# Performance work log

Hardware: AMD Instinct MI355X
Metric: run time of the kernel (lower is better)

Reference implementation:

```python
import jax, jax.numpy as jnp
import numpy as np

SCALE = 1.0 / 7.0
EPS = 1e-7


def _pair_iou(b1, b2):
    """Elementwise IoU of cxcywh boxes, faithful to Loss.bboxs_iou (incl. eps placement)."""
    b1x1 = b1[..., 0] - b1[..., 2] * 0.5
    b1x2 = b1[..., 0] + b1[..., 2] * 0.5
    b1y1 = b1[..., 1] - b1[..., 3] * 0.5
    b1y2 = b1[..., 1] + b1[..., 3] * 0.5
    b2x1 = b2[..., 0] - b2[..., 2] * 0.5
    b2x2 = b2[..., 0] + b2[..., 2] * 0.5
    b2y1 = b2[..., 1] - b2[..., 3] * 0.5
    b2y2 = b2[..., 1] + b2[..., 3] * 0.5
    iw = jnp.maximum(jnp.minimum(b1x2, b2x2) - jnp.maximum(b1x1, b2x1), 0.0)
    ih = jnp.maximum(jnp.minimum(b1y2, b2y2) - jnp.maximum(b1y1, b2y1), 0.0)
    inter = iw * ih + EPS
    w1 = b1x2 - b1x1
    h1 = b1y2 - b1y1 + EPS
    w2 = b2x2 - b2x1
    h2 = b2y2 - b2y1 + EPS
    union = w1 * h1 + w2 * h2 - inter + EPS
    return inter / union


def _msum(mask, sq):
    return jnp.sum(jnp.where(mask, sq, 0.0))


def _forward(pre, target):
    B = pre.shape[0]
    pre = pre.reshape(B, 7, 7, 30)
    cell_obj = target[..., 4] > 0       # (B,7,7) grid cells with an object
    cell_noobj = target[..., 4] == 0    # (B,7,7) empty cells

    t_box = target[..., :10].reshape(B, 7, 7, 2, 5)
    p_box = pre[..., :10].reshape(B, 7, 7, 2, 5)

    # per-cell, per-box IoU(pred_b, target_b), b in {0,1}  -> (B,7,7,2)
    iou = _pair_iou(p_box[..., :4], t_box[..., :4])
    resp = jnp.argmax(iou, axis=-1)      # responsible box index (first max, like torch)
    nonresp = jnp.argmin(iou, axis=-1)   # non-responsible box index (first min)

    box_idx = jnp.arange(2)[None, None, None, :]       # (1,1,1,2)
    is_resp = box_idx == resp[..., None]               # (B,7,7,2)
    is_nonresp = box_idx == nonresp[..., None]

    # loop effect 1: zero the confidence of the non-responsible TARGET box
    new_conf = jnp.where(is_nonresp, 0.0, t_box[..., 4])   # (B,7,7,2)

    # loop effect 2: responsible target xy <- normalized offset of the *min-index* box's xy
    xy_nr = jnp.take_along_axis(t_box[..., :2], nonresp[..., None, None], axis=3)  # (B,7,7,1,2)
    xy_nr = xy_nr[..., 0, :]                                                        # (B,7,7,2)
    fxy = (xy_nr - (jnp.ceil(xy_nr / SCALE) - 1.0) * SCALE) / SCALE                 # (B,7,7,2)
    new_xy = jnp.where(is_resp[..., None], fxy[:, :, :, None, :], t_box[..., :2])   # (B,7,7,2,2)

    m_resp = is_resp & cell_obj[..., None]        # responsible boxes of object cells
    m_noresp = (~is_resp) & cell_obj[..., None]   # nomse mask (init 1, cleared at resp)

    loss_xy = _msum(m_resp[..., None], (p_box[..., :2] - new_xy) ** 2)
    loss_wh = _msum(m_resp[..., None],
                    (jnp.sqrt(p_box[..., 2:4] + EPS) - jnp.sqrt(t_box[..., 2:4] + EPS)) ** 2)
    loss_conf = _msum(m_resp, (p_box[..., 4] - new_conf) ** 2)
    loss_noconf = (_msum(m_noresp, (p_box[..., 4] - new_conf) ** 2)
                   + _msum(cell_noobj[..., None], (p_box[..., 4] - t_box[..., 4]) ** 2))
    loss_class = _msum(cell_obj[..., None], (pre[..., 10:] - target[..., 10:]) ** 2)

    loss = 5.0 * (loss_xy + loss_wh) + loss_class + loss_conf + 0.5 * loss_noconf
    return loss / jnp.float32(B)


def setup_inputs() -> dict:
    key = jax.random.key(0)
    k1, k2, k3 = jax.random.split(key, 3)
    B = 16384
    pre = jax.random.uniform(k1, (B, 7 * 7 * 30), dtype=jnp.float32)
    target = jax.random.uniform(k2, (B, 7, 7, 30), dtype=jnp.float32)
    # objectness in {0,1} on both box conf channels so obj/no-obj branches are exercised
    obj = (jax.random.uniform(k3, (B, 7, 7)) > 0.5).astype(jnp.float32)
    target = target.at[..., 4].set(obj).at[..., 9].set(obj)
    return {"pre": pre, "target": target}


def reference(pre, target):
    return _forward(pre, target)
```

## Files before the change

kernel.cpp:

```cpp
#include <hip/hip_runtime.h>

#define EPSF 1e-7f
#define SCALEF (1.0f / 7.0f)

__device__ __forceinline__ float pair_iou(const float* b1, const float* b2) {
    float b1x1 = b1[0] - b1[2] * 0.5f, b1x2 = b1[0] + b1[2] * 0.5f;
    float b1y1 = b1[1] - b1[3] * 0.5f, b1y2 = b1[1] + b1[3] * 0.5f;
    float b2x1 = b2[0] - b2[2] * 0.5f, b2x2 = b2[0] + b2[2] * 0.5f;
    float b2y1 = b2[1] - b2[3] * 0.5f, b2y2 = b2[1] + b2[3] * 0.5f;
    float iw = fmaxf(fminf(b1x2, b2x2) - fmaxf(b1x1, b2x1), 0.0f);
    float ih = fmaxf(fminf(b1y2, b2y2) - fmaxf(b1y1, b2y1), 0.0f);
    float inter = iw * ih + EPSF;
    float w1 = b1x2 - b1x1, h1 = b1y2 - b1y1 + EPSF;
    float w2 = b2x2 - b2x1, h2 = b2y2 - b2y1 + EPSF;
    float uni = w1 * h1 + w2 * h2 - inter + EPSF;
    return inter / uni;
}

__global__ __launch_bounds__(256) void yolo_loss_partial(
        const float* __restrict__ pre, const float* __restrict__ targ,
        float* __restrict__ partial, int n_cells) {
    int cell = blockIdx.x * 256 + threadIdx.x;
    float loss = 0.0f;
    if (cell < n_cells) {
        float p[30], t[30];
        const float2* p2 = reinterpret_cast<const float2*>(pre + (size_t)cell * 30);
        const float2* t2 = reinterpret_cast<const float2*>(targ + (size_t)cell * 30);
#pragma unroll
        for (int i = 0; i < 15; ++i) { float2 v = p2[i]; p[2 * i] = v.x; p[2 * i + 1] = v.y; }
#pragma unroll
        for (int i = 0; i < 15; ++i) { float2 v = t2[i]; t[2 * i] = v.x; t[2 * i + 1] = v.y; }

        bool cell_obj   = t[4] > 0.0f;
        bool cell_noobj = t[4] == 0.0f;

        float iou0 = pair_iou(p + 0, t + 0);
        float iou1 = pair_iou(p + 5, t + 5);
        int resp    = (iou1 > iou0) ? 1 : 0;
        int nonresp = (iou1 < iou0) ? 1 : 0;

        float xnr = nonresp ? t[5] : t[0];
        float ynr = nonresp ? t[6] : t[1];
        float fx = (xnr - (ceilf(xnr / SCALEF) - 1.0f) * SCALEF) / SCALEF;
        float fy = (ynr - (ceilf(ynr / SCALEF) - 1.0f) * SCALEF) / SCALEF;

        float lxy = 0.0f, lwh = 0.0f, lconf = 0.0f, lnoconf = 0.0f, lclass = 0.0f;
#pragma unroll
        for (int i = 0; i < 2; ++i) {
            const float* pb = p + i * 5;
            const float* tb = t + i * 5;
            bool is_resp    = (i == resp);
            bool is_nonresp = (i == nonresp);
            float new_conf = is_nonresp ? 0.0f : tb[4];
            if (cell_obj) {
                if (is_resp) {
                    float dx = pb[0] - fx, dy = pb[1] - fy;
                    lxy += dx * dx + dy * dy;
                    float dw = sqrtf(pb[2] + EPSF) - sqrtf(tb[2] + EPSF);
                    float dh = sqrtf(pb[3] + EPSF) - sqrtf(tb[3] + EPSF);
                    lwh += dw * dw + dh * dh;
                    float dc = pb[4] - new_conf;
                    lconf += dc * dc;
                } else {
                    float dc = pb[4] - new_conf;
                    lnoconf += dc * dc;
                }
            }
            if (cell_noobj) {
                float dc = pb[4] - tb[4];
                lnoconf += dc * dc;
            }
        }
        if (cell_obj) {
#pragma unroll
            for (int k = 10; k < 30; ++k) { float d = p[k] - t[k]; lclass += d * d; }
        }
        loss = 5.0f * (lxy + lwh) + lclass + lconf + 0.5f * lnoconf;
    }

#pragma unroll
    for (int off = 32; off > 0; off >>= 1) loss += __shfl_down(loss, off, 64);
    __shared__ float ssum[4];
    int lane = threadIdx.x & 63, wid = threadIdx.x >> 6;
    if (lane == 0) ssum[wid] = loss;
    __syncthreads();
    if (threadIdx.x == 0) partial[blockIdx.x] = ssum[0] + ssum[1] + ssum[2] + ssum[3];
}

__global__ __launch_bounds__(256) void yolo_loss_final(
        const float* __restrict__ partial, int n, float invB, float* __restrict__ out) {
    float v = 0.0f;
    for (int i = threadIdx.x; i < n; i += 256) v += partial[i];
#pragma unroll
    for (int off = 32; off > 0; off >>= 1) v += __shfl_down(v, off, 64);
    __shared__ float ssum[4];
    int lane = threadIdx.x & 63, wid = threadIdx.x >> 6;
    if (lane == 0) ssum[wid] = v;
    __syncthreads();
    if (threadIdx.x == 0) out[0] = (ssum[0] + ssum[1] + ssum[2] + ssum[3]) * invB;
}

extern "C" void kernel_launch(void* const* d_in, const int* in_sizes, int n_in,
                              void* d_out, int out_size, void* d_ws, size_t ws_size,
                              hipStream_t stream) {
    const float* pre  = (const float*)d_in[0];
    const float* targ = (const float*)d_in[1];
    float* out = (float*)d_out;
    float* partial = (float*)d_ws;

    int B = in_sizes[0] / 1470;
    int n_cells = B * 49;
    int nblocks = (n_cells + 255) / 256;

    yolo_loss_partial<<<nblocks, 256, 0, stream>>>(pre, targ, partial, n_cells);
    yolo_loss_final<<<1, 256, 0, stream>>>(partial, nblocks, 1.0f / (float)B, out);
}
```

Baseline: 44.33 us.

## Stage cells through LDS with coalesced float4 loads and split box/class work

Each block copies 128 cells of pred and target into shared memory with coalesced float4 loads, two chunks per block. Half the threads then compute the box/IoU terms and the other half the class term, which balances work and cuts per-thread registers. The aim is to replace strided per-thread float2 global loads (stride of 120 bytes) with fully coalesced transfers. The bounds check is removed and the grid is floor-divided, which assumes n_cells is a multiple of 256. That holds for B=16384 but is not a general guarantee.

```diff
diff --git a/kernel.cpp b/kernel.cpp
--- a/kernel.cpp
+++ b/kernel.cpp
@@ -19,72 +19,110 @@
 
 __global__ __launch_bounds__(256) void yolo_loss_partial(
         const float* __restrict__ pre, const float* __restrict__ targ,
-        float* __restrict__ partial, int n_cells) {
-    int cell = blockIdx.x * 256 + threadIdx.x;
-    float loss = 0.0f;
-    if (cell < n_cells) {
-        float p[30], t[30];
-        const float2* p2 = reinterpret_cast<const float2*>(pre + (size_t)cell * 30);
-        const float2* t2 = reinterpret_cast<const float2*>(targ + (size_t)cell * 30);
+        float* __restrict__ partial) {
+    __shared__ float4 s4[1920];
+    float* sp = reinterpret_cast<float*>(s4);
+    float* st = reinterpret_cast<float*>(s4 + 960);
+    const int tid = threadIdx.x;
+    float acc = 0.0f;
+
 #pragma unroll
-        for (int i = 0; i < 15; ++i) { float2 v = p2[i]; p[2 * i] = v.x; p[2 * i + 1] = v.y; }
+    for (int chunk = 0; chunk < 2; ++chunk) {
+        const size_t base = ((size_t)blockIdx.x * 256 + chunk * 128) * 30;
+        const float4* gp = reinterpret_cast<const float4*>(pre + base);
+        const float4* gt = reinterpret_cast<const float4*>(targ + base);
+        float4* sp4 = s4;
+        float4* st4 = s4 + 960;
 #pragma unroll
-        for (int i = 0; i < 15; ++i) { float2 v = t2[i]; t[2 * i] = v.x; t[2 * i + 1] = v.y; }
+        for (int k = 0; k < 3; ++k) {
+            int idx = tid + 256 * k;
+            sp4[idx] = gp[idx];
+            st4[idx] = gt[idx];
+        }
+        {
+            int idx = tid + 768;
+            if (idx < 960) { sp4[idx] = gp[idx]; st4[idx] = gt[idx]; }
+        }
+        __syncthreads();
 
-        bool cell_obj   = t[4] > 0.0f;
-        bool cell_noobj = t[4] == 0.0f;
-
-        float iou0 = pair_iou(p + 0, t + 0);
-        float iou1 = pair_iou(p + 5, t + 5);
-        int resp    = (iou1 > iou0) ? 1 : 0;
-        int nonresp = (iou1 < iou0) ? 1 : 0;
-
-        float xnr = nonresp ? t[5] : t[0];
-        float ynr = nonresp ? t[6] : t[1];
-        float fx = (xnr - (ceilf(xnr / SCALEF) - 1.0f) * SCALEF) / SCALEF;
-        float fy = (ynr - (ceilf(ynr / SCALEF) - 1.0f) * SCALEF) / SCALEF;
-
-        float lxy = 0.0f, lwh = 0.0f, lconf = 0.0f, lnoconf = 0.0f, lclass = 0.0f;
+        const int half = tid >> 7;
+        const int c = tid & 127;
+        const float* cp = sp + c * 30;
+        const float* ct = st + c * 30;
+        float loss = 0.0f;
+        if (half == 0) {
+            float p[10], t[10];
+            const float2* cp2 = reinterpret_cast<const float2*>(cp);
+            const float2* ct2 = reinterpret_cast<const float2*>(ct);
 #pragma unroll
-        for (int i = 0; i < 2; ++i) {
-            const float* pb = p + i * 5;
-            const float* tb = t + i * 5;
-            bool is_resp    = (i == resp);
-            bool is_nonresp = (i == nonresp);
-            float new_conf = is_nonresp ? 0.0f : tb[4];
-            if (cell_obj) {
-                if (is_resp) {
-                    float dx = pb[0] - fx, dy = pb[1] - fy;
-                    lxy += dx * dx + dy * dy;
-                    float dw = sqrtf(pb[2] + EPSF) - sqrtf(tb[2] + EPSF);
-                    float dh = sqrtf(pb[3] + EPSF) - sqrtf(tb[3] + EPSF);
-                    lwh += dw * dw + dh * dh;
-                    float dc = pb[4] - new_conf;
-                    lconf += dc * dc;
-                } else {
-                    float dc = pb[4] - new_conf;
+            for (int i = 0; i < 5; ++i) {
+                float2 a = cp2[i]; p[2 * i] = a.x; p[2 * i + 1] = a.y;
+                float2 b = ct2[i]; t[2 * i] = b.x; t[2 * i + 1] = b.y;
+            }
+            bool cell_obj   = t[4] > 0.0f;
+            bool cell_noobj = t[4] == 0.0f;
+            float iou0 = pair_iou(p + 0, t + 0);
+            float iou1 = pair_iou(p + 5, t + 5);
+            int resp    = (iou1 > iou0) ? 1 : 0;
+            int nonresp = (iou1 < iou0) ? 1 : 0;
+            float xnr = nonresp ? t[5] : t[0];
+            float ynr = nonresp ? t[6] : t[1];
+            float fx = (xnr - (ceilf(xnr / SCALEF) - 1.0f) * SCALEF) / SCALEF;
+            float fy = (ynr - (ceilf(ynr / SCALEF) - 1.0f) * SCALEF) / SCALEF;
+            float lxy = 0.0f, lwh = 0.0f, lconf = 0.0f, lnoconf = 0.0f;
+#pragma unroll
+            for (int i = 0; i < 2; ++i) {
+                const float* pb = p + i * 5;
+                const float* tb = t + i * 5;
+                bool is_resp    = (i == resp);
+                bool is_nonresp = (i == nonresp);
+                float new_conf = is_nonresp ? 0.0f : tb[4];
+                if (cell_obj) {
+                    if (is_resp) {
+                        float dx = pb[0] - fx, dy = pb[1] - fy;
+                        lxy += dx * dx + dy * dy;
+                        float dw = sqrtf(pb[2] + EPSF) - sqrtf(tb[2] + EPSF);
+                        float dh = sqrtf(pb[3] + EPSF) - sqrtf(tb[3] + EPSF);
+                        lwh += dw * dw + dh * dh;
+                        float dc = pb[4] - new_conf;
+                        lconf += dc * dc;
+                    } else {
+                        float dc = pb[4] - new_conf;
+                        lnoconf += dc * dc;
+                    }
+                }
+                if (cell_noobj) {
+                    float dc = pb[4] - tb[4];
                     lnoconf += dc * dc;
                 }
             }
-            if (cell_noobj) {
-                float dc = pb[4] - tb[4];
-                lnoconf += dc * dc;
+            loss = 5.0f * (lxy + lwh) + lconf + 0.5f * lnoconf;
+        } else {
+            float tobj = ct[4];
+            if (tobj > 0.0f) {
+                float s = 0.0f;
+                const float2* cp2 = reinterpret_cast<const float2*>(cp + 10);
+                const float2* ct2 = reinterpret_cast<const float2*>(ct + 10);
+#pragma unroll
+                for (int i = 0; i < 10; ++i) {
+                    float2 a = cp2[i], b = ct2[i];
+                    float d0 = a.x - b.x, d1 = a.y - b.y;
+                    s += d0 * d0 + d1 * d1;
+                }
+                loss = s;
             }
         }
-        if (cell_obj) {
-#pragma unroll
-            for (int k = 10; k < 30; ++k) { float d = p[k] - t[k]; lclass += d * d; }
-        }
-        loss = 5.0f * (lxy + lwh) + lclass + lconf + 0.5f * lnoconf;
+        acc += loss;
+        __syncthreads();
     }
 
 #pragma unroll
-    for (int off = 32; off > 0; off >>= 1) loss += __shfl_down(loss, off, 64);
+    for (int off = 32; off > 0; off >>= 1) acc += __shfl_down(acc, off, 64);
     __shared__ float ssum[4];
-    int lane = threadIdx.x & 63, wid = threadIdx.x >> 6;
-    if (lane == 0) ssum[wid] = loss;
+    int lane = tid & 63, wid = tid >> 6;
+    if (lane == 0) ssum[wid] = acc;
     __syncthreads();
-    if (threadIdx.x == 0) partial[blockIdx.x] = ssum[0] + ssum[1] + ssum[2] + ssum[3];
+    if (tid == 0) partial[blockIdx.x] = ssum[0] + ssum[1] + ssum[2] + ssum[3];
 }
 
 __global__ __launch_bounds__(256) void yolo_loss_final(
@@ -110,8 +148,8 @@
 
     int B = in_sizes[0] / 1470;
     int n_cells = B * 49;
-    int nblocks = (n_cells + 255) / 256;
+    int nblocks = n_cells / 256;
 
-    yolo_loss_partial<<<nblocks, 256, 0, stream>>>(pre, targ, partial, n_cells);
+    yolo_loss_partial<<<nblocks, 256, 0, stream>>>(pre, targ, partial);
     yolo_loss_final<<<1, 256, 0, stream>>>(partial, nblocks, 1.0f / (float)B, out);
 }
```

Result: faster. 37.96 us (median of 2 runs) (-14.4%).
